# Performance work log

Measured on AMD Instinct MI355X. Metric: run time of the kernel, lower is better.

## Reference

```python
import jax, jax.numpy as jnp
import numpy as np

N_NODES = 100000
N_EDGES = 1600000
N_GRAPHS = 128
IN_CH, OUT_CH, N_CLASS = 768, 128, 2


def setup_inputs() -> dict:
    key = jax.random.key(0)
    ks = jax.random.split(key, 8)
    x = jax.random.normal(ks[0], (N_NODES, IN_CH), dtype=jnp.float32)
    # directed edges with src < dst so to_undirected (concat + reverse) has no duplicates
    src = jax.random.randint(ks[1], (N_EDGES,), 0, N_NODES - 1, dtype=jnp.int32)
    dst = jax.random.randint(ks[2], (N_EDGES,), 1, N_NODES, dtype=jnp.int32)
    dst = jnp.where(dst <= src, src + 1, dst)  # ensure src < dst (no self-loops)
    edge_index = jnp.stack([src, dst], axis=0)
    batch = jnp.sort(jax.random.randint(ks[3], (N_NODES,), 0, N_GRAPHS, dtype=jnp.int32))
    s = 0.05
    return {
        "x": x,
        "edge_index": edge_index,
        "batch": batch,
        "num_graphs": N_GRAPHS,
        "W_conv": jax.random.normal(ks[4], (IN_CH, OUT_CH), dtype=jnp.float32) * s,
        "b_conv": jnp.zeros((OUT_CH,), dtype=jnp.float32),
        "W_lin0": jax.random.normal(ks[5], (IN_CH, OUT_CH), dtype=jnp.float32) * s,
        "b_lin0": jnp.zeros((OUT_CH,), dtype=jnp.float32),
        "W_lin1": jax.random.normal(ks[6], (2 * OUT_CH, OUT_CH), dtype=jnp.float32) * s,
        "b_lin1": jnp.zeros((OUT_CH,), dtype=jnp.float32),
        "W_lin2": jax.random.normal(ks[7], (OUT_CH, N_CLASS), dtype=jnp.float32) * s,
        "b_lin2": jnp.zeros((N_CLASS,), dtype=jnp.float32),
    }


def _gcn_conv(x, W, b, src, dst, n_nodes):
    # GCNConv: linear transform, add self-loops, symmetric normalization, scatter-add
    loop = jnp.arange(n_nodes, dtype=src.dtype)
    s = jnp.concatenate([src, loop])
    d = jnp.concatenate([dst, loop])
    deg = jax.ops.segment_sum(jnp.ones_like(d, dtype=x.dtype), d, num_segments=n_nodes)
    dinv = jnp.where(deg > 0, jax.lax.rsqrt(deg), 0.0)
    norm = dinv[s] * dinv[d]  # [E']
    h = x @ W  # [N, out]
    msg = h[s] * norm[:, None]  # gather + scale
    return jax.ops.segment_sum(msg, d, num_segments=n_nodes) + b


def reference(x, edge_index, batch, num_graphs, W_conv, b_conv,
              W_lin0, b_lin0, W_lin1, b_lin1, W_lin2, b_lin2):
    n_nodes = x.shape[0]
    # to_undirected: add reversed edges (input has src<dst so no duplicates to coalesce)
    src = jnp.concatenate([edge_index[0], edge_index[1]])
    dst = jnp.concatenate([edge_index[1], edge_index[0]])
    h = jax.nn.relu(_gcn_conv(x, W_conv, b_conv, src, dst, n_nodes))
    # global max pool over graphs
    h = jax.ops.segment_max(h, batch, num_segments=num_graphs)  # [G, out]
    # root node = first node of each graph (batch is sorted)
    root = jax.ops.segment_min(jnp.arange(n_nodes), batch, num_segments=num_graphs)
    news = jax.nn.relu(x[root] @ W_lin0 + b_lin0)  # [G, out]
    h = jax.nn.relu(jnp.concatenate([news, h], axis=-1) @ W_lin1 + b_lin1)
    logits = h @ W_lin2 + b_lin2
    return jax.nn.log_softmax(logits, axis=-1)
```

## Files before the change

kernel.cpp:

```cpp
#include <hip/hip_runtime.h>

#define N_NODES 100000
#define N_EDGES 1600000
#define N_GRAPHS 128
#define IN_CH 768
#define OUT_CH 128

#define BSHIFT 8
#define NBKT ((N_NODES + 255) / 256)
#define EPB 2000
#define CAPREC 16384
#define PADV 16
#define CAPADJ (CAPREC + 256 * (PADV - 1))

using short8 = __attribute__((ext_vector_type(8))) short;
using f32x4  = __attribute__((ext_vector_type(4))) float;

__device__ __forceinline__ float bf2f(unsigned short u) {
    return __uint_as_float(((unsigned)u) << 16);
}
__device__ __forceinline__ unsigned short f2bf(float f) {
    unsigned u = __float_as_uint(f);
    u += 0x7fffu + ((u >> 16) & 1u);
    return (unsigned short)(u >> 16);
}
__device__ __forceinline__ float load_f(const void* p, size_t i, int f32) {
    return f32 ? ((const float*)p)[i] : bf2f(((const unsigned short*)p)[i]);
}
__device__ __forceinline__ float lo16(unsigned p) { return __uint_as_float(p << 16); }
__device__ __forceinline__ float hi16(unsigned p) { return __uint_as_float(p & 0xffff0000u); }

__global__ void k_init(int* flag, int* gcur, unsigned* pooled, int* root,
                       const int* __restrict__ batch, const unsigned short* __restrict__ xbits,
                       const void* Wc, const void* bc, const void* W0, const void* b0,
                       const void* W1, const void* b1, const void* W2, const void* b2,
                       unsigned short* Wt, float* fbc, float* fW0, float* fb0,
                       float* fW1, float* fb1, float* fW2, float* fb2) {
    __shared__ int sflag;
    if (threadIdx.x == 0) sflag = 0;
    __syncthreads();
    int bad = 0;
    for (int j = threadIdx.x; j < 8192; j += 256) {
        float v = bf2f(xbits[j]);
        if (!(v > -64.f && v < 64.f)) bad = 1;
    }
    if (bad) atomicOr(&sflag, 1);
    __syncthreads();
    int f32 = sflag;
    int i = blockIdx.x * blockDim.x + threadIdx.x;
    if (i == 0) *flag = f32;
    if (i < NBKT) gcur[i] = i * CAPREC;
    if (i < N_GRAPHS * OUT_CH) pooled[i] = 0u;
    if (i < N_NODES) {
        int b = batch[i];
        if (i == 0 || batch[i - 1] != b) root[b] = i;
    }
    if (i < IN_CH * OUT_CH) {
        int n = i / IN_CH, k = i - n * IN_CH;
        Wt[i] = f32 ? f2bf(((const float*)Wc)[k * OUT_CH + n])
                    : ((const unsigned short*)Wc)[k * OUT_CH + n];
        fW0[i] = load_f(W0, i, f32);
    }
    if (i < 2 * OUT_CH * OUT_CH) fW1[i] = load_f(W1, i, f32);
    if (i < OUT_CH * 2) fW2[i] = load_f(W2, i, f32);
    if (i < OUT_CH) { fbc[i] = load_f(bc, i, f32); fb0[i] = load_f(b0, i, f32); fb1[i] = load_f(b1, i, f32); }
    if (i < 2) fb2[i] = load_f(b2, i, f32);
}

__global__ __launch_bounds__(256) void k_bin(const int* __restrict__ src, const int* __restrict__ dst,
                                             int* gcur, unsigned* __restrict__ binned) {
    __shared__ int hist[NBKT];
    __shared__ int basep[NBKT];
    int t = threadIdx.x;
    for (int b = t; b < NBKT; b += 256) hist[b] = 0;
    __syncthreads();
    int e0 = blockIdx.x * EPB, e1 = e0 + EPB;
    if (e1 > N_EDGES) e1 = N_EDGES;
    for (int i = e0 + t; i < e1; i += 256) {
        unsigned s_ = (unsigned)src[i]; if (s_ >= N_NODES) s_ = N_NODES - 1u;
        unsigned d_ = (unsigned)dst[i]; if (d_ >= N_NODES) d_ = N_NODES - 1u;
        atomicAdd(&hist[d_ >> BSHIFT], 1);
        atomicAdd(&hist[s_ >> BSHIFT], 1);
    }
    __syncthreads();
    for (int b = t; b < NBKT; b += 256) {
        int c = hist[b];
        if (c) {
            int base = atomicAdd(&gcur[b], c);
            basep[b] = (base + c <= (b + 1) * CAPREC) ? base : -1;
        }
        hist[b] = 0;
    }
    __syncthreads();
    for (int i = e0 + t; i < e1; i += 256) {
        unsigned s_ = (unsigned)src[i]; if (s_ >= N_NODES) s_ = N_NODES - 1u;
        unsigned d_ = (unsigned)dst[i]; if (d_ >= N_NODES) d_ = N_NODES - 1u;
        unsigned bd = d_ >> BSHIFT, bs = s_ >> BSHIFT;
        int pd_ = basep[bd], ps_ = basep[bs];
        int od = atomicAdd(&hist[bd], 1);
        int os = atomicAdd(&hist[bs], 1);
        if (pd_ >= 0) binned[pd_ + od] = (s_ << 8) | (d_ & 255u);
        if (ps_ >= 0) binned[ps_ + os] = (d_ << 8) | (s_ & 255u);
    }
}

__global__ __launch_bounds__(256) void k_build(const unsigned* __restrict__ binned,
                                               const int* __restrict__ gcur,
                                               int2* odeg, float* dinv, int* adj) {
    __shared__ int sdeg[256], scur[256], sscan[256];
    int b = blockIdx.x, t = threadIdx.x;
    int base = b * CAPREC;
    int n = gcur[b] - base;
    if (n > CAPREC) n = CAPREC;
    if (n < 0) n = 0;
    int base_adj = b * CAPADJ;
    sdeg[t] = 0;
    __syncthreads();
    int npair = n & ~1;
    for (int j = t * 2; j < npair; j += 512) {
        uint2 rr = *(const uint2*)&binned[base + j];
        atomicAdd(&sdeg[rr.x & 255u], 1);
        atomicAdd(&sdeg[rr.y & 255u], 1);
    }
    if ((n & 1) && t == 0) atomicAdd(&sdeg[binned[base + n - 1] & 255u], 1);
    __syncthreads();
    int myd = sdeg[t];
    int pd = (myd + PADV - 1) & ~(PADV - 1);
    sscan[t] = pd;
    __syncthreads();
    for (int off = 1; off < 256; off <<= 1) {
        int add = (t >= off) ? sscan[t - off] : 0;
        __syncthreads();
        sscan[t] += add;
        __syncthreads();
    }
    int excl = sscan[t] - pd;
    int node = (b << BSHIFT) + t;
    if (node < N_NODES) {
        odeg[node] = make_int2(base_adj + excl, pd);
        dinv[node] = rsqrtf((float)(myd + 1));
    }
    for (int j = myd; j < pd; j++) adj[base_adj + excl + j] = N_NODES;
    scur[t] = excl;
    __syncthreads();
    for (int j = t * 2; j < npair; j += 512) {
        uint2 rr = *(const uint2*)&binned[base + j];
        adj[base_adj + atomicAdd(&scur[rr.x & 255u], 1)] = (int)(rr.x >> 8);
        adj[base_adj + atomicAdd(&scur[rr.y & 255u], 1)] = (int)(rr.y >> 8);
    }
    if ((n & 1) && t == 0) {
        unsigned rec = binned[base + n - 1];
        adj[base_adj + atomicAdd(&scur[rec & 255u], 1)] = (int)(rec >> 8);
    }
}

#define MBLK 128
#define BK 64
#define LSTR 72

__global__ __launch_bounds__(256) void k_gemm(const int* __restrict__ flag,
                                              const void* __restrict__ xv,
                                              const unsigned short* __restrict__ Wt,
                                              const float* __restrict__ dinv,
                                              unsigned short* __restrict__ h) {
    __shared__ __align__(16) unsigned short As[MBLK * LSTR];
    __shared__ __align__(16) unsigned short Bs[OUT_CH * LSTR];
    const int f32 = *flag;
    const int tid = threadIdx.x;
    if (blockIdx.x == 0 && tid < 64) ((unsigned*)(h + (size_t)N_NODES * OUT_CH))[tid] = 0u;
    const int wave = tid >> 6, lane = tid & 63;
    const int quad = lane >> 4, l16 = lane & 15;
    const int wm = (wave >> 1) * 64, wn = (wave & 1) * 64;
    const int row0 = blockIdx.x * MBLK;

    f32x4 acc[4][4];
#pragma unroll
    for (int mt = 0; mt < 4; mt++)
#pragma unroll
        for (int nt = 0; nt < 4; nt++) acc[mt][nt] = (f32x4){0.f, 0.f, 0.f, 0.f};

    int r_[4], c8_[4];
    size_t arow_[4];
#pragma unroll
    for (int i = 0; i < 4; i++) {
        int chunk = tid + i * 256;
        r_[i] = chunk >> 3;
        c8_[i] = (chunk & 7) << 3;
        int gr = row0 + r_[i]; if (gr >= N_NODES) gr = N_NODES - 1;
        arow_[i] = (size_t)gr * IN_CH;
    }

    float4 fa[4][2];
    uint4  ua[4];
    uint4  rb[4];

#define LOADK(K0)                                                                      \
    {                                                                                  \
        if (f32) {                                                                     \
            _Pragma("unroll") for (int i = 0; i < 4; i++) {                            \
                const float* xp = (const float*)xv + arow_[i] + (K0) + c8_[i];         \
                fa[i][0] = *(const float4*)xp;                                         \
                fa[i][1] = *(const float4*)(xp + 4);                                   \
            }                                                                          \
        } else {                                                                       \
            _Pragma("unroll") for (int i = 0; i < 4; i++)                              \
                ua[i] = *(const uint4*)((const unsigned short*)xv + arow_[i] + (K0) + c8_[i]); \
        }                                                                              \
        _Pragma("unroll") for (int i = 0; i < 4; i++)                                  \
            rb[i] = *(const uint4*)(Wt + (size_t)r_[i] * IN_CH + (K0) + c8_[i]);       \
    }

#define STOREK()                                                                       \
    {                                                                                  \
        if (f32) {                                                                     \
            _Pragma("unroll") for (int i = 0; i < 4; i++) {                            \
                uint4 va;                                                              \
                va.x = (unsigned)f2bf(fa[i][0].x) | ((unsigned)f2bf(fa[i][0].y) << 16);\
                va.y = (unsigned)f2bf(fa[i][0].z) | ((unsigned)f2bf(fa[i][0].w) << 16);\
                va.z = (unsigned)f2bf(fa[i][1].x) | ((unsigned)f2bf(fa[i][1].y) << 16);\
                va.w = (unsigned)f2bf(fa[i][1].z) | ((unsigned)f2bf(fa[i][1].w) << 16);\
                *(uint4*)&As[r_[i] * LSTR + c8_[i]] = va;                              \
                *(uint4*)&Bs[r_[i] * LSTR + c8_[i]] = rb[i];                           \
            }                                                                          \
        } else {                                                                       \
            _Pragma("unroll") for (int i = 0; i < 4; i++) {                            \
                *(uint4*)&As[r_[i] * LSTR + c8_[i]] = ua[i];                           \
                *(uint4*)&Bs[r_[i] * LSTR + c8_[i]] = rb[i];                           \
            }                                                                          \
        }                                                                              \
    }

#define COMPUTE()                                                                      \
    {                                                                                  \
        _Pragma("unroll") for (int kk = 0; kk < BK; kk += 32) {                        \
            short8 af[4], bf[4];                                                       \
            _Pragma("unroll") for (int mt = 0; mt < 4; mt++)                           \
                af[mt] = *(const short8*)&As[(wm + mt * 16 + l16) * LSTR + kk + quad * 8]; \
            _Pragma("unroll") for (int nt = 0; nt < 4; nt++)                           \
                bf[nt] = *(const short8*)&Bs[(wn + nt * 16 + l16) * LSTR + kk + quad * 8]; \
            _Pragma("unroll") for (int mt = 0; mt < 4; mt++)                           \
                _Pragma("unroll") for (int nt = 0; nt < 4; nt++)                       \
                    acc[mt][nt] = __builtin_amdgcn_mfma_f32_16x16x32_bf16(af[mt], bf[nt], acc[mt][nt], 0, 0, 0); \
        }                                                                              \
    }

    LOADK(0);
    STOREK();
    __syncthreads();
    LOADK(BK);
    for (int k0 = 0;; k0 += BK) {
        COMPUTE();
        int kn = k0 + BK;
        if (kn >= IN_CH) break;
        __syncthreads();
        STOREK();
        if (kn + BK < IN_CH) LOADK(kn + BK);
        __syncthreads();
    }

#pragma unroll
    for (int mt = 0; mt < 4; mt++) {
#pragma unroll
        for (int r = 0; r < 4; r++) {
            int m = row0 + wm + mt * 16 + quad * 4 + r;
            if (m >= N_NODES) continue;
            float dvm = dinv[m];
#pragma unroll
            for (int nt = 0; nt < 4; nt++) {
                int col = wn + nt * 16 + l16;
                h[(size_t)m * OUT_CH + col] = f2bf(acc[mt][nt][r] * dvm);
            }
        }
    }
#undef LOADK
#undef STOREK
#undef COMPUTE
}

__global__ __launch_bounds__(256) void k_agg(const unsigned short* __restrict__ h,
                                             const int* __restrict__ adj,
                                             const int2* __restrict__ odeg,
                                             const float* __restrict__ dinv,
                                             const int* __restrict__ batch,
                                             const float* __restrict__ fbc,
                                             unsigned* pooled) {
    int wave = threadIdx.x >> 6, lane = threadIdx.x & 63;
    int node = blockIdx.x * 4 + wave;
    float dv = dinv[node];
    int l16 = lane & 15;

    uint4 own = *(const uint4*)(h + (size_t)node * OUT_CH + l16 * 8);
    float gsel = (lane < 16) ? 1.f : 0.f;
    float a0 = lo16(own.x) * gsel, a1 = hi16(own.x) * gsel;
    float a2 = lo16(own.y) * gsel, a3 = hi16(own.y) * gsel;
    float a4 = lo16(own.z) * gsel, a5 = hi16(own.z) * gsel;
    float a6 = lo16(own.w) * gsel, a7 = hi16(own.w) * gsel;

    int2 od = odeg[node];
    int o = od.x, e = od.x + od.y;
#define GATH(q)                                                              \
    {                                                                        \
        unsigned rlo = (lane & 16) ? (q).y : (q).x;                          \
        unsigned rhi = (lane & 16) ? (q).w : (q).z;                          \
        unsigned row = (lane & 32) ? rhi : rlo;                              \
        uint4 pv = *(const uint4*)(h + (size_t)row * OUT_CH + l16 * 8);      \
        a0 += lo16(pv.x); a1 += hi16(pv.x);                                  \
        a2 += lo16(pv.y); a3 += hi16(pv.y);                                  \
        a4 += lo16(pv.z); a5 += hi16(pv.z);                                  \
        a6 += lo16(pv.w); a7 += hi16(pv.w);                                  \
    }
    int i = o;
    for (; i + 32 <= e; i += 32) {
        uint4 q0 = *(const uint4*)&adj[i];
        uint4 q1 = *(const uint4*)&adj[i + 4];
        uint4 q2 = *(const uint4*)&adj[i + 8];
        uint4 q3 = *(const uint4*)&adj[i + 12];
        uint4 q4 = *(const uint4*)&adj[i + 16];
        uint4 q5 = *(const uint4*)&adj[i + 20];
        uint4 q6 = *(const uint4*)&adj[i + 24];
        uint4 q7 = *(const uint4*)&adj[i + 28];
        GATH(q0) GATH(q1) GATH(q2) GATH(q3)
        GATH(q4) GATH(q5) GATH(q6) GATH(q7)
    }
    for (; i < e; i += 16) {
        uint4 q0 = *(const uint4*)&adj[i];
        uint4 q1 = *(const uint4*)&adj[i + 4];
        uint4 q2 = *(const uint4*)&adj[i + 8];
        uint4 q3 = *(const uint4*)&adj[i + 12];
        GATH(q0) GATH(q1) GATH(q2) GATH(q3)
    }
#undef GATH

    a0 += __shfl_xor(a0, 16, 64); a1 += __shfl_xor(a1, 16, 64);
    a2 += __shfl_xor(a2, 16, 64); a3 += __shfl_xor(a3, 16, 64);
    a4 += __shfl_xor(a4, 16, 64); a5 += __shfl_xor(a5, 16, 64);
    a6 += __shfl_xor(a6, 16, 64); a7 += __shfl_xor(a7, 16, 64);
    a0 += __shfl_xor(a0, 32, 64); a1 += __shfl_xor(a1, 32, 64);
    a2 += __shfl_xor(a2, 32, 64); a3 += __shfl_xor(a3, 32, 64);
    a4 += __shfl_xor(a4, 32, 64); a5 += __shfl_xor(a5, 32, 64);
    a6 += __shfl_xor(a6, 32, 64); a7 += __shfl_xor(a7, 32, 64);

    float4 bA = *(const float4*)&fbc[l16 * 8];
    float4 bB = *(const float4*)&fbc[l16 * 8 + 4];
    float r0 = fmaxf(fmaf(a0, dv, bA.x), 0.f);
    float r1 = fmaxf(fmaf(a1, dv, bA.y), 0.f);
    float r2 = fmaxf(fmaf(a2, dv, bA.z), 0.f);
    float r3 = fmaxf(fmaf(a3, dv, bA.w), 0.f);
    float r4 = fmaxf(fmaf(a4, dv, bB.x), 0.f);
    float r5 = fmaxf(fmaf(a5, dv, bB.y), 0.f);
    float r6 = fmaxf(fmaf(a6, dv, bB.z), 0.f);
    float r7 = fmaxf(fmaf(a7, dv, bB.w), 0.f);

    int g = batch[node];
    __shared__ float s0[256], s1[256];
    __shared__ int sg[4];
    if (lane < 16) {
        *(float4*)&s0[wave * 64 + l16 * 4] = (float4){r0, r2, r4, r6};
        *(float4*)&s1[wave * 64 + l16 * 4] = (float4){r1, r3, r5, r7};
        if (l16 == 0) sg[wave] = g;
    }
    __syncthreads();
    if (wave == 0) {
        int g0 = sg[0];
        if (sg[1] == g0 && sg[2] == g0 && sg[3] == g0) {
            float m0 = fmaxf(fmaxf(s0[lane], s0[64 + lane]), fmaxf(s0[128 + lane], s0[192 + lane]));
            float m1 = fmaxf(fmaxf(s1[lane], s1[64 + lane]), fmaxf(s1[128 + lane], s1[192 + lane]));
            atomicMax(&pooled[g0 * OUT_CH + lane * 2],     __float_as_uint(m0));
            atomicMax(&pooled[g0 * OUT_CH + lane * 2 + 1], __float_as_uint(m1));
        } else {
#pragma unroll
            for (int w = 0; w < 4; w++) {
                atomicMax(&pooled[sg[w] * OUT_CH + lane * 2],     __float_as_uint(s0[w * 64 + lane]));
                atomicMax(&pooled[sg[w] * OUT_CH + lane * 2 + 1], __float_as_uint(s1[w * 64 + lane]));
            }
        }
    }
}

__global__ __launch_bounds__(256) void k_final(const int* __restrict__ flag,
                                               const void* __restrict__ x,
                                               const int* __restrict__ root,
                                               const unsigned* __restrict__ pooled,
                                               const float* __restrict__ W0,
                                               const float* __restrict__ b0,
                                               const float* __restrict__ W1,
                                               const float* __restrict__ b1,
                                               const float* __restrict__ W2,
                                               const float* __restrict__ b2,
                                               void* out) {
    __shared__ float xs[IN_CH];
    __shared__ float ps[256];
    __shared__ float ins[2 * OUT_CH];
    __shared__ float h2s[OUT_CH];
    int f32 = *flag;
    int g = blockIdx.x, t = threadIdx.x;
    int r = root[g]; if ((unsigned)r >= N_NODES) r = 0;
    for (int j = t; j < IN_CH; j += 256) xs[j] = load_f(x, (size_t)r * IN_CH + j, f32);
    if (t >= 128) ins[OUT_CH + (t - 128)] = __uint_as_float(pooled[g * OUT_CH + (t - 128)]);
    __syncthreads();
    {
        int c = t & 127, half = t >> 7;
        int k0 = half * (IN_CH / 2);
        float acc = 0.f;
#pragma unroll 8
        for (int k = 0; k < IN_CH / 2; k++) acc += xs[k0 + k] * W0[(size_t)(k0 + k) * OUT_CH + c];
        ps[t] = acc;
    }
    __syncthreads();
    if (t < 128) ins[t] = fmaxf(ps[t] + ps[t + 128] + b0[t], 0.f);
    __syncthreads();
    {
        int c = t & 127, half = t >> 7;
        int k0 = half * OUT_CH;
        float acc = 0.f;
#pragma unroll 8
        for (int k = 0; k < OUT_CH; k++) acc += ins[k0 + k] * W1[(size_t)(k0 + k) * OUT_CH + c];
        ps[t] = acc;
    }
    __syncthreads();
    if (t < 128) h2s[t] = fmaxf(ps[t] + ps[t + 128] + b1[t], 0.f);
    __syncthreads();
    if (t == 0) {
        float l0 = b2[0], l1 = b2[1];
        for (int k = 0; k < OUT_CH; k++) { float v = h2s[k]; l0 += v * W2[k * 2]; l1 += v * W2[k * 2 + 1]; }
        float m = fmaxf(l0, l1);
        float ls = m + logf(expf(l0 - m) + expf(l1 - m));
        if (f32) {
            ((float*)out)[g * 2]     = l0 - ls;
            ((float*)out)[g * 2 + 1] = l1 - ls;
        } else {
            ((unsigned short*)out)[g * 2]     = f2bf(l0 - ls);
            ((unsigned short*)out)[g * 2 + 1] = f2bf(l1 - ls);
        }
    }
}

extern "C" void kernel_launch(void* const* d_in, const int* in_sizes, int n_in,
                              void* d_out, int out_size, void* d_ws, size_t ws_size,
                              hipStream_t stream) {
    const void* x     = d_in[0];
    const int*  ei    = (const int*)d_in[1];
    const int*  batch = (const int*)d_in[2];
    const void* Wc    = d_in[4];
    const void* bc    = d_in[5];
    const void* W0    = d_in[6];
    const void* b0    = d_in[7];
    const void* W1    = d_in[8];
    const void* b1    = d_in[9];
    const void* W2    = d_in[10];
    const void* b2    = d_in[11];
    const int* src = ei;
    const int* dst = ei + N_EDGES;

    char* p = (char*)d_ws;
    auto carve = [&](size_t bytes) -> void* {
        void* r = (void*)p;
        p += (bytes + 255) & ~(size_t)255;
        return r;
    };
    int*      flag      = (int*)carve(4);
    int*      gcur      = (int*)carve((size_t)NBKT * 4);
    int2*     odeg      = (int2*)carve((size_t)N_NODES * 8);
    float*    dinv      = (float*)carve((size_t)N_NODES * 4);
    int*      root      = (int*)carve(128 * 4);
    unsigned* pooled    = (unsigned*)carve((size_t)N_GRAPHS * OUT_CH * 4);
    unsigned short* Wt  = (unsigned short*)carve((size_t)IN_CH * OUT_CH * 2);
    float*    fW0       = (float*)carve((size_t)IN_CH * OUT_CH * 4);
    float*    fW1       = (float*)carve((size_t)2 * OUT_CH * OUT_CH * 4);
    float*    fW2       = (float*)carve((size_t)OUT_CH * 2 * 4);
    float*    fbc       = (float*)carve((size_t)OUT_CH * 4);
    float*    fb0       = (float*)carve((size_t)OUT_CH * 4);
    float*    fb1       = (float*)carve((size_t)OUT_CH * 4);
    float*    fb2       = (float*)carve(2 * 4);
    int*      adj       = (int*)carve((size_t)NBKT * CAPADJ * 4);
    size_t binned_bytes = (size_t)NBKT * CAPREC * 4;
    size_t h_bytes      = (size_t)(N_NODES + 1) * OUT_CH * 2;
    void*     hb        = carve(binned_bytes > h_bytes ? binned_bytes : h_bytes);
    unsigned* binned    = (unsigned*)hb;
    unsigned short* h   = (unsigned short*)hb;

    const int nEdgeBlk = (N_EDGES + EPB - 1) / EPB;

    k_init  <<<391, 256, 0, stream>>>(flag, gcur, pooled, root, batch, (const unsigned short*)x,
                                      Wc, bc, W0, b0, W1, b1, W2, b2,
                                      Wt, fbc, fW0, fb0, fW1, fb1, fW2, fb2);
    k_bin   <<<nEdgeBlk, 256, 0, stream>>>(src, dst, gcur, binned);
    k_build <<<NBKT, 256, 0, stream>>>(binned, gcur, odeg, dinv, adj);
    k_gemm  <<<(N_NODES + MBLK - 1) / MBLK, 256, 0, stream>>>(flag, x, Wt, dinv, h);
    k_agg   <<<N_NODES / 4, 256, 0, stream>>>(h, adj, odeg, dinv, batch, fbc, pooled);
    k_final <<<N_GRAPHS, 256, 0, stream>>>(flag, x, root, pooled, fW0, fb0, fW1, fb1, fW2, fb2, d_out);
}
```

Measured before the change: 690.3 us.

## Software-pipeline adjacency index loads and halve per-node padding in gather

The gather loop now prefetches the next 16 adjacency indices while gathering rows for the current 16, replacing the 32-wide unrolled loop. Per-node adjacency padding drops from 16 to 8 entries, with an 8-entry tail, which cuts wasted dummy-row gathers. EPB (edges per block in the build phase) is doubled. The risks are extra register pressure from the double-buffered indices, and a different block/capacity balance that must still fit within CAPADJ.

Measured after the change: 698.9 us. About the same (+1.2%).

```diff
diff --git a/kernel.cpp b/kernel.cpp
--- a/kernel.cpp
+++ b/kernel.cpp
@@ -8,9 +8,9 @@
 
 #define BSHIFT 8
 #define NBKT ((N_NODES + 255) / 256)
-#define EPB 2000
+#define EPB 4000
 #define CAPREC 16384
-#define PADV 16
+#define PADV 8
 #define CAPADJ (CAPREC + 256 * (PADV - 1))
 
 using short8 = __attribute__((ext_vector_type(8))) short;
@@ -310,24 +310,31 @@
         a6 += lo16(pv.w); a7 += hi16(pv.w);                                  \
     }
     int i = o;
-    for (; i + 32 <= e; i += 32) {
-        uint4 q0 = *(const uint4*)&adj[i];
-        uint4 q1 = *(const uint4*)&adj[i + 4];
-        uint4 q2 = *(const uint4*)&adj[i + 8];
-        uint4 q3 = *(const uint4*)&adj[i + 12];
-        uint4 q4 = *(const uint4*)&adj[i + 16];
-        uint4 q5 = *(const uint4*)&adj[i + 20];
-        uint4 q6 = *(const uint4*)&adj[i + 24];
-        uint4 q7 = *(const uint4*)&adj[i + 28];
-        GATH(q0) GATH(q1) GATH(q2) GATH(q3)
-        GATH(q4) GATH(q5) GATH(q6) GATH(q7)
-    }
-    for (; i < e; i += 16) {
-        uint4 q0 = *(const uint4*)&adj[i];
-        uint4 q1 = *(const uint4*)&adj[i + 4];
-        uint4 q2 = *(const uint4*)&adj[i + 8];
-        uint4 q3 = *(const uint4*)&adj[i + 12];
-        GATH(q0) GATH(q1) GATH(q2) GATH(q3)
+    int e16 = o + ((e - o) & ~15);
+    if (i < e16) {
+        uint4 c0 = *(const uint4*)&adj[i];
+        uint4 c1 = *(const uint4*)&adj[i + 4];
+        uint4 c2 = *(const uint4*)&adj[i + 8];
+        uint4 c3 = *(const uint4*)&adj[i + 12];
+        for (;;) {
+            int nx = i + 16;
+            uint4 n0 = c0, n1 = c1, n2 = c2, n3 = c3;
+            if (nx < e16) {
+                n0 = *(const uint4*)&adj[nx];
+                n1 = *(const uint4*)&adj[nx + 4];
+                n2 = *(const uint4*)&adj[nx + 8];
+                n3 = *(const uint4*)&adj[nx + 12];
+            }
+            GATH(c0) GATH(c1) GATH(c2) GATH(c3)
+            i = nx;
+            if (i >= e16) break;
+            c0 = n0; c1 = n1; c2 = n2; c3 = n3;
+        }
+    }
+    if (i < e) {
+        uint4 t0 = *(const uint4*)&adj[i];
+        uint4 t1 = *(const uint4*)&adj[i + 4];
+        GATH(t0) GATH(t1)
     }
 #undef GATH
 
```
